# Optimization experiments

Hardware: AMD Instinct MI355X
Metric: run time of the kernel (lower is better)

The kernel has to match this reference:

```python
import jax, jax.numpy as jnp
import numpy as np


def _segment_sparsemax(x, batch, B):
    """Per-group sparsemax over a flat ragged tensor.

    x: [N] float values; batch: [N] sorted int group ids in [0, B).
    Groups are contiguous, so an in-group descending sort is a stable
    lexsort on (batch, -x); per-group cumsum is a global cumsum minus the
    cumsum value just before each group's start offset.
    """
    N = x.shape[0]
    num_nodes = jax.ops.segment_sum(jnp.ones(N, jnp.int32), batch, num_segments=B)  # [B]
    start = jnp.concatenate([jnp.zeros(1, jnp.int32), jnp.cumsum(num_nodes)[:-1]])  # [B]

    # shift by per-group max for numerical stability (as in torch forward)
    gmax = jax.ops.segment_max(x, batch, num_segments=B)
    xs = x - gmax[batch]

    # descending sort within each contiguous group
    order = jnp.lexsort((-xs, batch))
    sx = xs[order]  # [N], group-wise descending; group layout unchanged

    # per-group cumulative sum via global cumsum + start offsets
    cs = jnp.cumsum(sx)
    off = jnp.where(start > 0, cs[jnp.maximum(start - 1, 0)], jnp.zeros((), sx.dtype))  # [B]
    seg_cs = cs - off[batch] - 1.0  # input_cumsum - 1.0

    # rho = 1..n_g within each group
    rho = (jnp.arange(N, dtype=jnp.int32) - start[batch] + 1).astype(xs.dtype)

    support = rho * sx > seg_cs  # [N] bool
    supp_size = jax.ops.segment_sum(support.astype(jnp.int32), batch, num_segments=B)  # [B]

    idx = jnp.maximum(supp_size + start - 1, 0)  # [B]
    tau = seg_cs[idx] / supp_size.astype(xs.dtype)  # [B]

    return jnp.maximum(xs - tau[batch], 0.0)


def setup_inputs() -> dict:
    key = jax.random.key(0)
    k1, k2 = jax.random.split(key)
    N = 8_388_608
    B = 4096
    x = jax.random.normal(k1, (N,), dtype=jnp.float32)
    batch = jnp.sort(jax.random.randint(k2, (N,), 0, B)).astype(jnp.int64)
    return {"x": x, "batch": batch, "num_groups": B}


def reference(x, batch, num_groups):
    batch = batch.astype(jnp.int32)
    return _segment_sparsemax(x, batch, int(num_groups))
```

## Files before the change

### kernel.cpp

```cpp
#include <hip/hip_runtime.h>

#define BLK 256
#define WPB 4
#define RPT4 12
#define CAPW (RPT4 * 64 * 4)
#define CCAP 72


__device__ __forceinline__ float wave_max(float v) {
#pragma unroll
  for (int o = 32; o; o >>= 1) v = fmaxf(v, __shfl_xor(v, o));
  return v;
}
__device__ __forceinline__ float wave_sum(float v) {
#pragma unroll
  for (int o = 32; o; o >>= 1) v += __shfl_xor(v, o);
  return v;
}
__device__ __forceinline__ int wave_sum_i(int v) {
#pragma unroll
  for (int o = 32; o; o >>= 1) v += __shfl_xor(v, o);
  return v;
}


extern "C" __global__ void __launch_bounds__(256)
build_starts(const int* __restrict__ batch, int* __restrict__ starts,
             const int* __restrict__ pB, int N) {
  const int B = *pB;
  const long long tid = (long long)blockIdx.x * 256 + threadIdx.x;
  const long long i0 = tid * 8;
  if (i0 >= N) return;
  int v[8];
  if (i0 + 8 <= N) {
    const int4 a = *(const int4*)(batch + i0);
    const int4 b = *(const int4*)(batch + i0 + 4);
    v[0] = a.x; v[1] = a.y; v[2] = a.z; v[3] = a.w;
    v[4] = b.x; v[5] = b.y; v[6] = b.z; v[7] = b.w;
  } else {
#pragma unroll
    for (int t = 0; t < 8; ++t) v[t] = (i0 + t < N) ? batch[i0 + t] : 0;
  }
  int prev = (i0 == 0) ? -1 : batch[i0 - 1];
#pragma unroll
  for (int t = 0; t < 8; ++t) {
    if (i0 + t >= N) break;
    const int cur = v[t];
    for (int g = prev + 1; g <= cur; ++g) starts[g] = (int)(i0 + t);
    prev = cur;
  }
  if (i0 + 8 >= N) {
    for (int g = prev + 1; g <= B; ++g) starts[g] = N;
  }
}


extern "C" __global__ void __launch_bounds__(BLK)
sparsemax_groups(const float* __restrict__ x, const int* __restrict__ starts,
                 const int* __restrict__ pB, float* __restrict__ out, int N) {
  __shared__ float cand[WPB][CCAP];
  __shared__ float sorted[WPB][CCAP];
  __shared__ int   cnt[WPB];
  const int lane = threadIdx.x & 63;
  const int w    = threadIdx.x >> 6;
  const int B = *pB;
  const int wstride = gridDim.x * WPB;

  for (int g = blockIdx.x * WPB + w; g < B; g += wstride) {
    const int s = starts[g];
    const int e = starts[g + 1];
    const int n = e - s;
    if (n <= 0) continue;
    const int a0 = s & ~3;

    if (e - a0 <= CAPW) {
      float4 r[RPT4];
      float gmax = -INFINITY;
#pragma unroll
      for (int j = 0; j < RPT4; ++j) {
        const int idx = a0 + (j * 64 + lane) * 4;
        float4 v = make_float4(-INFINITY, -INFINITY, -INFINITY, -INFINITY);
        if (idx < e) {
          if (idx + 4 <= N) {
            v = *(const float4*)(x + idx);
          } else {
            if (idx + 0 < N) v.x = x[idx + 0];
            if (idx + 1 < N) v.y = x[idx + 1];
            if (idx + 2 < N) v.z = x[idx + 2];
            if (idx + 3 < N) v.w = x[idx + 3];
          }
          if (idx + 0 < s || idx + 0 >= e) v.x = -INFINITY;
          if (idx + 1 < s || idx + 1 >= e) v.y = -INFINITY;
          if (idx + 2 < s || idx + 2 >= e) v.z = -INFINITY;
          if (idx + 3 < s || idx + 3 >= e) v.w = -INFINITY;
        }
        r[j] = v;
        gmax = fmaxf(gmax, fmaxf(fmaxf(v.x, v.y), fmaxf(v.z, v.w)));
      }
      gmax = wave_max(gmax);

      if (lane == 0) cnt[w] = 0;
      const float thr = gmax - 1.0f;
      float csum = 0.0f; int cm = 0;
#pragma unroll
      for (int j = 0; j < RPT4; ++j) {
        const float vv[4] = {r[j].x, r[j].y, r[j].z, r[j].w};
#pragma unroll
        for (int t = 0; t < 4; ++t) {
          if (vv[t] > thr) {
            const int p = atomicAdd(&cnt[w], 1);
            if (p < CCAP) cand[w][p] = vv[t];
            csum += vv[t] - gmax; cm++;
          }
        }
      }
      const int c = wave_sum_i(cm);

      float tau;
      if (c <= 64) {
        const float v = (lane < c) ? cand[w][lane] - gmax : 0.0f;
        int rank = 0;
        for (int q = 0; q < c; ++q) {
          const float t = cand[w][q] - gmax;
          rank += (t > v) || (t == v && q < lane);
        }
        if (lane < c) sorted[w][rank] = v;
        const float sv = (lane < c) ? sorted[w][lane] : 0.0f;
        float cs = sv;
#pragma unroll
        for (int o = 1; o < 64; o <<= 1) {
          const float t = __shfl_up(cs, o);
          if (lane >= o) cs += t;
        }
        const int flag = (lane < c) && (sv * (float)(lane + 1) > cs - 1.0f);
        const unsigned long long bal = __ballot(flag);
        const int k = 63 - __clzll(bal);
        const float csk = __shfl(cs, k);
        tau = (csk - 1.0f) / (float)(k + 1);
      } else {
        float bs = wave_sum(csum); int bc = c;
        tau = (bs - 1.0f) / (float)bc;
        for (int it = 0; it < 64; ++it) {
          float s2 = 0.0f; int c2 = 0;
#pragma unroll
          for (int j = 0; j < RPT4; ++j) {
            const float vv[4] = {r[j].x, r[j].y, r[j].z, r[j].w};
#pragma unroll
            for (int t = 0; t < 4; ++t) {
              const float vs = vv[t] - gmax;
              if (vs > tau) { s2 += vs; c2++; }
            }
          }
          s2 = wave_sum(s2); c2 = wave_sum_i(c2);
          if (c2 == bc || c2 == 0) break;
          tau = (s2 - 1.0f) / (float)c2; bc = c2;
        }
      }

      const float sub = tau + gmax;
#pragma unroll
      for (int j = 0; j < RPT4; ++j) {
        const int idx = a0 + (j * 64 + lane) * 4;
        if (idx >= e) continue;
        if (idx >= s && idx + 4 <= e) {
          float4 o4;
          o4.x = fmaxf(r[j].x - sub, 0.0f);
          o4.y = fmaxf(r[j].y - sub, 0.0f);
          o4.z = fmaxf(r[j].z - sub, 0.0f);
          o4.w = fmaxf(r[j].w - sub, 0.0f);
          *(float4*)(out + idx) = o4;
        } else {
          const float vv[4] = {r[j].x, r[j].y, r[j].z, r[j].w};
#pragma unroll
          for (int t = 0; t < 4; ++t) {
            const int p = idx + t;
            if (p >= s && p < e) out[p] = fmaxf(vv[t] - sub, 0.0f);
          }
        }
      }
    } else {
      float gmax = -INFINITY;
      for (int i = s + lane; i < e; i += 64) gmax = fmaxf(gmax, x[i]);
      gmax = wave_max(gmax);
      float bs = 0.0f; int bc = 0;
      for (int i = s + lane; i < e; i += 64) {
        const float vs = x[i] - gmax;
        if (vs > -1.0f) { bs += vs; bc++; }
      }
      bs = wave_sum(bs); bc = wave_sum_i(bc);
      float tau = (bs - 1.0f) / (float)bc;
      int cntS = bc;
      for (int it = 0; it < 64; ++it) {
        float s2 = 0.0f; int c2 = 0;
        for (int i = s + lane; i < e; i += 64) {
          const float vs = x[i] - gmax;
          if (vs > tau) { s2 += vs; c2++; }
        }
        s2 = wave_sum(s2); c2 = wave_sum_i(c2);
        if (c2 == cntS || c2 == 0) break;
        tau = (s2 - 1.0f) / (float)c2; cntS = c2;
      }
      const float sub = tau + gmax;
      for (int i = s + lane; i < e; i += 64) out[i] = fmaxf(x[i] - sub, 0.0f);
    }
  }
}

extern "C" void kernel_launch(void* const* d_in, const int* in_sizes, int n_in,
                              void* d_out, int out_size, void* d_ws, size_t ws_size,
                              hipStream_t stream) {
  const float* x     = (const float*)d_in[0];
  const int*   batch = (const int*)d_in[1];
  const int*   pB    = (const int*)d_in[2];
  float*       out   = (float*)d_out;
  const int N = in_sizes[0];

  int* starts = (int*)d_ws;

  const int g1 = (N + 2047) / 2048;
  build_starts<<<dim3(g1), dim3(256), 0, stream>>>(batch, starts, pB, N);
  sparsemax_groups<<<dim3(1024), dim3(BLK), 0, stream>>>(x, starts, pB, out, N);
}
```

Baseline: 117.7 us.

## Process each group with a whole block instead of one wave

Each segment is now handled by a 256-thread block instead of a single wavefront. Register tiling drops from 12 float4 per lane to 3, and candidate collection uses wave-aggregated ballot atomics into a shared buffer. A new middle path runs the threshold iteration on shared candidates, and the grid grows to 4096 blocks, one per group. The aim is to cut per-thread register pressure and the serial per-wave work, which should raise occupancy. In exchange it adds block-level syncs and shared-memory reductions for every group.

```diff
diff --git a/kernel.cpp b/kernel.cpp
--- a/kernel.cpp
+++ b/kernel.cpp
@@ -1,10 +1,9 @@
 #include <hip/hip_runtime.h>
 
 #define BLK 256
-#define WPB 4
-#define RPT4 12
-#define CAPW (RPT4 * 64 * 4)
-#define CCAP 72
+#define QPT 3
+#define CAPB (QPT * BLK * 4)
+#define CCAP 320
 
 
 __device__ __forceinline__ float wave_max(float v) {
@@ -21,6 +20,15 @@
 #pragma unroll
   for (int o = 32; o; o >>= 1) v += __shfl_xor(v, o);
   return v;
+}
+
+__device__ __forceinline__ void block_sum_cnt(float& s, int& c, float* redf, int* redi, int tid) {
+  s = wave_sum(s); c = wave_sum_i(c);
+  __syncthreads();
+  if ((tid & 63) == 0) { redf[tid >> 6] = s; redi[tid >> 6] = c; }
+  __syncthreads();
+  s = redf[0] + redf[1] + redf[2] + redf[3];
+  c = redi[0] + redi[1] + redi[2] + redi[3];
 }
 
 
@@ -58,27 +66,31 @@
 extern "C" __global__ void __launch_bounds__(BLK)
 sparsemax_groups(const float* __restrict__ x, const int* __restrict__ starts,
                  const int* __restrict__ pB, float* __restrict__ out, int N) {
-  __shared__ float cand[WPB][CCAP];
-  __shared__ float sorted[WPB][CCAP];
-  __shared__ int   cnt[WPB];
-  const int lane = threadIdx.x & 63;
-  const int w    = threadIdx.x >> 6;
+  __shared__ float redf[4];
+  __shared__ int   redi[4];
+  __shared__ float cand[CCAP];
+  __shared__ float sorted[64];
+  __shared__ int   s_cnt;
+  __shared__ float s_csum;
+  __shared__ float s_tau;
+  const int tid  = threadIdx.x;
+  const int lane = tid & 63;
+  const int w    = tid >> 6;
   const int B = *pB;
-  const int wstride = gridDim.x * WPB;
-
-  for (int g = blockIdx.x * WPB + w; g < B; g += wstride) {
+
+  for (int g = blockIdx.x; g < B; g += gridDim.x) {
     const int s = starts[g];
     const int e = starts[g + 1];
     const int n = e - s;
     if (n <= 0) continue;
     const int a0 = s & ~3;
 
-    if (e - a0 <= CAPW) {
-      float4 r[RPT4];
-      float gmax = -INFINITY;
-#pragma unroll
-      for (int j = 0; j < RPT4; ++j) {
-        const int idx = a0 + (j * 64 + lane) * 4;
+    if (e - a0 <= CAPB) {
+      float4 r[QPT];
+      float lmax = -INFINITY;
+#pragma unroll
+      for (int j = 0; j < QPT; ++j) {
+        const int idx = a0 + (j * BLK + tid) * 4;
         float4 v = make_float4(-INFINITY, -INFINITY, -INFINITY, -INFINITY);
         if (idx < e) {
           if (idx + 4 <= N) {
@@ -95,55 +107,85 @@
           if (idx + 3 < s || idx + 3 >= e) v.w = -INFINITY;
         }
         r[j] = v;
-        gmax = fmaxf(gmax, fmaxf(fmaxf(v.x, v.y), fmaxf(v.z, v.w)));
-      }
-      gmax = wave_max(gmax);
-
-      if (lane == 0) cnt[w] = 0;
+        lmax = fmaxf(lmax, fmaxf(fmaxf(v.x, v.y), fmaxf(v.z, v.w)));
+      }
+      lmax = wave_max(lmax);
+      if (lane == 0) redf[w] = lmax;
+      if (tid == 0) { s_cnt = 0; s_csum = 0.0f; }
+      __syncthreads();
+      const float gmax = fmaxf(fmaxf(redf[0], redf[1]), fmaxf(redf[2], redf[3]));
       const float thr = gmax - 1.0f;
-      float csum = 0.0f; int cm = 0;
-#pragma unroll
-      for (int j = 0; j < RPT4; ++j) {
+
+      float wsum = 0.0f;
+#pragma unroll
+      for (int j = 0; j < QPT; ++j) {
         const float vv[4] = {r[j].x, r[j].y, r[j].z, r[j].w};
 #pragma unroll
         for (int t = 0; t < 4; ++t) {
-          if (vv[t] > thr) {
-            const int p = atomicAdd(&cnt[w], 1);
-            if (p < CCAP) cand[w][p] = vv[t];
-            csum += vv[t] - gmax; cm++;
-          }
-        }
-      }
-      const int c = wave_sum_i(cm);
-
-      float tau;
+          const bool p = vv[t] > thr;
+          const unsigned long long bal = __ballot(p);
+          if (bal) {
+            int base = 0;
+            if (lane == 0) base = atomicAdd(&s_cnt, __popcll(bal));
+            base = __shfl(base, 0);
+            if (p) {
+              const int off = base + __popcll(bal & ((1ull << lane) - 1ull));
+              if (off < CCAP) cand[off] = vv[t];
+              wsum += vv[t] - gmax;
+            }
+          }
+        }
+      }
+      wsum = wave_sum(wsum);
+      if (lane == 0) atomicAdd(&s_csum, wsum);
+      __syncthreads();
+      const int c = s_cnt;
+
       if (c <= 64) {
-        const float v = (lane < c) ? cand[w][lane] - gmax : 0.0f;
-        int rank = 0;
-        for (int q = 0; q < c; ++q) {
-          const float t = cand[w][q] - gmax;
-          rank += (t > v) || (t == v && q < lane);
-        }
-        if (lane < c) sorted[w][rank] = v;
-        const float sv = (lane < c) ? sorted[w][lane] : 0.0f;
-        float cs = sv;
-#pragma unroll
-        for (int o = 1; o < 64; o <<= 1) {
-          const float t = __shfl_up(cs, o);
-          if (lane >= o) cs += t;
-        }
-        const int flag = (lane < c) && (sv * (float)(lane + 1) > cs - 1.0f);
-        const unsigned long long bal = __ballot(flag);
-        const int k = 63 - __clzll(bal);
-        const float csk = __shfl(cs, k);
-        tau = (csk - 1.0f) / (float)(k + 1);
+        if (w == 0) {
+          const float v = (lane < c) ? cand[lane] - gmax : 0.0f;
+          int rank = 0;
+          for (int q = 0; q < c; ++q) {
+            const float t = cand[q] - gmax;
+            rank += (t > v) || (t == v && q < lane);
+          }
+          if (lane < c) sorted[rank] = v;
+          const float sv = (lane < c) ? sorted[lane] : 0.0f;
+          float cs = sv;
+#pragma unroll
+          for (int o = 1; o < 64; o <<= 1) {
+            const float t2 = __shfl_up(cs, o);
+            if (lane >= o) cs += t2;
+          }
+          const int flag = (lane < c) && (sv * (float)(lane + 1) > cs - 1.0f);
+          const unsigned long long bal2 = __ballot(flag);
+          const int k = 63 - __clzll(bal2);
+          const float csk = __shfl(cs, k);
+          if (lane == 0) s_tau = (csk - 1.0f) / (float)(k + 1);
+        }
+      } else if (c <= CCAP) {
+        if (w == 0) {
+          float tau = (s_csum - 1.0f) / (float)c;
+          int cnt = c;
+          for (int it = 0; it < 64; ++it) {
+            float s2 = 0.0f; int c2 = 0;
+            for (int q = lane; q < c; q += 64) {
+              const float vs = cand[q] - gmax;
+              if (vs > tau) { s2 += vs; c2++; }
+            }
+            s2 = wave_sum(s2); c2 = wave_sum_i(c2);
+            if (c2 == cnt || c2 == 0) break;
+            tau = (s2 - 1.0f) / (float)c2; cnt = c2;
+          }
+          if (lane == 0) s_tau = tau;
+        }
       } else {
-        float bs = wave_sum(csum); int bc = c;
-        tau = (bs - 1.0f) / (float)bc;
+        float tau = (s_csum - 1.0f) / (float)c;
+        int cnt = c;
         for (int it = 0; it < 64; ++it) {
           float s2 = 0.0f; int c2 = 0;
 #pragma unroll
-          for (int j = 0; j < RPT4; ++j) {
+          for (int j = 0; j < QPT; ++j) {
             const float vv[4] = {r[j].x, r[j].y, r[j].z, r[j].w};
 #pragma unroll
             for (int t = 0; t < 4; ++t) {
@@ -151,16 +193,18 @@
               if (vs > tau) { s2 += vs; c2++; }
             }
           }
-          s2 = wave_sum(s2); c2 = wave_sum_i(c2);
-          if (c2 == bc || c2 == 0) break;
-          tau = (s2 - 1.0f) / (float)c2; bc = c2;
-        }
-      }
-
-      const float sub = tau + gmax;
-#pragma unroll
-      for (int j = 0; j < RPT4; ++j) {
-        const int idx = a0 + (j * 64 + lane) * 4;
+          block_sum_cnt(s2, c2, redf, redi, tid);
+          if (c2 == cnt || c2 == 0) break;
+          tau = (s2 - 1.0f) / (float)c2; cnt = c2;
+        }
+        if (tid == 0) s_tau = tau;
+      }
+      __syncthreads();
+      const float sub = s_tau + gmax;
+
+#pragma unroll
+      for (int j = 0; j < QPT; ++j) {
+        const int idx = a0 + (j * BLK + tid) * 4;
         if (idx >= e) continue;
         if (idx >= s && idx + 4 <= e) {
           float4 o4;
@@ -173,35 +217,38 @@
           const float vv[4] = {r[j].x, r[j].y, r[j].z, r[j].w};
 #pragma unroll
           for (int t = 0; t < 4; ++t) {
-            const int p = idx + t;
-            if (p >= s && p < e) out[p] = fmaxf(vv[t] - sub, 0.0f);
+            const int p2 = idx + t;
+            if (p2 >= s && p2 < e) out[p2] = fmaxf(vv[t] - sub, 0.0f);
           }
         }
       }
     } else {
       float gmax = -INFINITY;
-      for (int i = s + lane; i < e; i += 64) gmax = fmaxf(gmax, x[i]);
+      for (int i = s + tid; i < e; i += BLK) gmax = fmaxf(gmax, x[i]);
       gmax = wave_max(gmax);
+      if (lane == 0) redf[w] = gmax;
+      __syncthreads();
+      gmax = fmaxf(fmaxf(redf[0], redf[1]), fmaxf(redf[2], redf[3]));
       float bs = 0.0f; int bc = 0;
-      for (int i = s + lane; i < e; i += 64) {
+      for (int i = s + tid; i < e; i += BLK) {
         const float vs = x[i] - gmax;
         if (vs > -1.0f) { bs += vs; bc++; }
       }
-      bs = wave_sum(bs); bc = wave_sum_i(bc);
+      block_sum_cnt(bs, bc, redf, redi, tid);
       float tau = (bs - 1.0f) / (float)bc;
       int cntS = bc;
       for (int it = 0; it < 64; ++it) {
         float s2 = 0.0f; int c2 = 0;
-        for (int i = s + lane; i < e; i += 64) {
+        for (int i = s + tid; i < e; i += BLK) {
           const float vs = x[i] - gmax;
           if (vs > tau) { s2 += vs; c2++; }
         }
-        s2 = wave_sum(s2); c2 = wave_sum_i(c2);
+        block_sum_cnt(s2, c2, redf, redi, tid);
         if (c2 == cntS || c2 == 0) break;
         tau = (s2 - 1.0f) / (float)c2; cntS = c2;
       }
       const float sub = tau + gmax;
-      for (int i = s + lane; i < e; i += 64) out[i] = fmaxf(x[i] - sub, 0.0f);
+      for (int i = s + tid; i < e; i += BLK) out[i] = fmaxf(x[i] - sub, 0.0f);
     }
   }
 }
@@ -219,5 +266,5 @@
 
   const int g1 = (N + 2047) / 2048;
   build_starts<<<dim3(g1), dim3(256), 0, stream>>>(batch, starts, pB, N);
-  sparsemax_groups<<<dim3(1024), dim3(BLK), 0, stream>>>(x, starts, pB, out, N);
-}
+  sparsemax_groups<<<dim3(4096), dim3(BLK), 0, stream>>>(x, starts, pB, out, N);
+}
```

New measurement: 111.9 us (median of 2 runs). 1.05x faster.
